# Kernel tuning notes

Measured on AMD Instinct MI355X. Metric: run time of the kernel, lower is better.

## Reference

```python
import jax, jax.numpy as jnp
import numpy as np

ALPHA = 0.5  # leakage
T, B, I, H = 512, 64, 128, 1024
SCALE = 0.9  # input_scaling
RHO = 0.99   # target spectral radius (approximated by 1/sqrt(H) normal scaling)


def setup_inputs() -> dict:
    key = jax.random.key(0)
    k1, k2, k3, k4, k5 = jax.random.split(key, 5)
    x = jax.random.normal(k1, (T, B, I), dtype=jnp.float32)
    # uniform(-scale, scale) kernel init
    W_in0 = jax.random.uniform(k2, (H, I), jnp.float32, -SCALE, SCALE)
    # normal recurrent init scaled so spectral radius ~= rho (circular law: radius ~ sigma*sqrt(H))
    W_hat0 = jax.random.normal(k3, (H, H), jnp.float32) * (RHO / np.sqrt(H))
    W_in1 = jax.random.uniform(k4, (H, H), jnp.float32, -SCALE, SCALE)
    W_hat1 = jax.random.normal(k5, (H, H), jnp.float32) * (RHO / np.sqrt(H))
    return {"x": x, "W_in0": W_in0, "W_hat0": W_hat0, "W_in1": W_in1, "W_hat1": W_hat1}


def _run_layer(inp, W_in, W_hat):
    # inp: [T, B, F_in]; returns full state trajectory [T, B, H]
    def step(h, x_t):
        pre = x_t @ W_in.T + h @ W_hat.T          # [B, H]
        h_new = (1.0 - ALPHA) * h + ALPHA * jnp.tanh(pre)
        return h_new, h_new

    h0 = jnp.zeros((inp.shape[1], W_hat.shape[0]), dtype=inp.dtype)
    _, ys = jax.lax.scan(step, h0, inp)
    return ys


def reference(x, W_in0, W_hat0, W_in1, W_hat1):
    e0 = _run_layer(x, W_in0, W_hat0)   # layer 0 states [T, B, H]
    e1 = _run_layer(e0, W_in1, W_hat1)  # layer 1 states [T, B, H]
    return jnp.stack([e0, e1], axis=-2)  # [T, B, num_layers, H]
```

## Files before the change

### kernel.cpp

```cpp
#include <hip/hip_runtime.h>
#include <math.h>

#define TSTEPS 512
#define BATCH  64
#define HDIM   1024
#define IDIM   128
#define NBLOCKS 256
#define NTHR   512

typedef __attribute__((ext_vector_type(8))) short bf16x8;
typedef __attribute__((ext_vector_type(4))) float f32x4;
typedef __attribute__((ext_vector_type(4))) unsigned u32x4;

#define WI0HI 0
#define WI0LO (WI0HI + 1024*128)
#define WH0HI (WI0LO + 1024*128)
#define WH0LO (WH0HI + 1024*1024)
#define WI1HI (WH0LO + 1024*1024)
#define WI1LO (WI1HI + 1024*1024)
#define WH1HI (WI1LO + 1024*1024)
#define WH1LO (WH1HI + 1024*1024)
#define WS_USHORTS (WH1LO + 1024*1024)
#define CNT_OFF_BYTES ((size_t)WS_USHORTS * 2)
#define BAR_BYTES (256 * 64)

__device__ __forceinline__ unsigned short bf_hi(float f) {
    unsigned u = __builtin_bit_cast(unsigned, f);
    unsigned r = u + 0x7fffu + ((u >> 16) & 1u);
    return (unsigned short)(r >> 16);
}
__device__ __forceinline__ float bf_tof(unsigned short h) {
    unsigned u = ((unsigned)h) << 16;
    return __builtin_bit_cast(float, u);
}

__device__ __forceinline__ void split8v(f32x4 a, f32x4 b,
                                        bf16x8& ah, bf16x8& al) {
    float fv[8] = {a[0], a[1], a[2], a[3], b[0], b[1], b[2], b[3]};
    u32x4 H, L;
    #pragma unroll
    for (int q = 0; q < 4; ++q) {
        const float f0 = fv[2 * q], f1 = fv[2 * q + 1];
        unsigned h;
        asm("v_cvt_pk_bf16_f32 %0, %1, %2" : "=v"(h) : "v"(f0), "v"(f1));
        const float h0 = __builtin_bit_cast(float, h << 16);
        const float h1 = __builtin_bit_cast(float, h & 0xffff0000u);
        unsigned lo;
        asm("v_cvt_pk_bf16_f32 %0, %1, %2" : "=v"(lo) : "v"(f0 - h0), "v"(f1 - h1));
        H[q] = h; L[q] = lo;
    }
    ah = __builtin_bit_cast(bf16x8, H);
    al = __builtin_bit_cast(bf16x8, L);
}

__device__ __forceinline__ void ks_r2(f32x4 a, f32x4 b,
                                      bf16x8 bh, bf16x8 bl, f32x4& acc) {
    bf16x8 ah, al;
    split8v(a, b, ah, al);
    acc = __builtin_amdgcn_mfma_f32_16x16x32_bf16(ah, bh, acc, 0, 0, 0);
    acc = __builtin_amdgcn_mfma_f32_16x16x32_bf16(al, bh, acc, 0, 0, 0);
    acc = __builtin_amdgcn_mfma_f32_16x16x32_bf16(ah, bl, acc, 0, 0, 0);
}

#define LD2(B, base, g) _Pragma("unroll") for (int c = 0; c < 2; ++c) { \
    (B)[2*c]   = *(const f32x4*)((base) + ((g)*2 + c) * 32); \
    (B)[2*c+1] = *(const f32x4*)((base) + ((g)*2 + c) * 32 + 4); }
#define PR2(B, wOff, g) _Pragma("unroll") for (int c = 0; c < 2; ++c) { \
    ks_r2((B)[2*c], (B)[2*c+1], wfh[(wOff)+(g)*2+c], wfl[(wOff)+(g)*2+c], \
          ((((g)*2+c) & 1) ? accA : accB)); }

__global__ void prep_kernel(const float* __restrict__ Wi0, const float* __restrict__ Wh0,
                            const float* __restrict__ Wi1, const float* __restrict__ Wh1,
                            unsigned short* __restrict__ wsU)
{
    const int n = 1024*128 + 3*1024*1024;
    for (int e = blockIdx.x * blockDim.x + threadIdx.x; e < n;
         e += gridDim.x * blockDim.x) {
        const float* src; int idx, hiOff, loOff;
        if (e < 1024*128)            { src = Wi0; idx = e;              hiOff = WI0HI; loOff = WI0LO; }
        else if (e < 1024*128 + 1024*1024)   { src = Wh0; idx = e - 1024*128;   hiOff = WH0HI; loOff = WH0LO; }
        else if (e < 1024*128 + 2*1024*1024) { src = Wi1; idx = e - 1024*128 - 1024*1024; hiOff = WI1HI; loOff = WI1LO; }
        else                         { src = Wh1; idx = e - 1024*128 - 2*1024*1024; hiOff = WH1HI; loOff = WH1LO; }
        float f = src[idx];
        unsigned short h = bf_hi(f);
        wsU[hiOff + idx] = h;
        wsU[loOff + idx] = bf_hi(f - bf_tof(h));
    }
}

__device__ __forceinline__ void barrier_arrive(unsigned* cnt, unsigned epoch,
                                               int dom, int jt) {
    __syncthreads();
    if (threadIdx.x == 0)
        __hip_atomic_store(cnt + (unsigned)(dom * 64 + jt) * 16, epoch,
                           __ATOMIC_RELAXED, __HIP_MEMORY_SCOPE_AGENT);
}
__device__ __forceinline__ void barrier_wait(unsigned* cnt, unsigned epoch,
                                             int layer, int mh) {
    const int tid = (int)threadIdx.x;
    if (tid < 64) {
        const int dom = layer * 2 + mh;
        unsigned* own = cnt + (unsigned)(dom * 64 + tid) * 16;
        if (layer == 0) {
            for (;;) {
                unsigned v = __hip_atomic_load(own, __ATOMIC_RELAXED,
                                               __HIP_MEMORY_SCOPE_AGENT);
                if (__ballot(v >= epoch) == ~0ull) break;
                __builtin_amdgcn_s_sleep(1);
            }
        } else {
            unsigned* up = cnt + (unsigned)(mh * 64 + tid) * 16;
            for (;;) {
                unsigned a = __hip_atomic_load(own, __ATOMIC_RELAXED,
                                               __HIP_MEMORY_SCOPE_AGENT);
                unsigned b = __hip_atomic_load(up, __ATOMIC_RELAXED,
                                               __HIP_MEMORY_SCOPE_AGENT);
                if (__ballot((a >= epoch) & (b >= epoch)) == ~0ull) break;
                __builtin_amdgcn_s_sleep(1);
            }
        }
    }
    __syncthreads();
}

__global__ __launch_bounds__(NTHR, 2) void reservoir_kernel(
    const float* __restrict__ x, float* __restrict__ out,
    const unsigned short* __restrict__ wsU, unsigned* __restrict__ cnt)
{
    __shared__ f32x4 red[8 * 64];

    const int bid = blockIdx.x;
    const int layer = bid >> 7;
    const int rr  = bid & 127;
    const int jt  = rr >> 1, mh = rr & 1;
    const int dom = layer * 2 + mh;
    const int tid = (int)threadIdx.x;
    const int w   = __builtin_amdgcn_readfirstlane(tid >> 6);
    const int m2  = w & 1, kh = w >> 1;
    const int l   = tid & 63, lr = l & 15, tq = l >> 4;
    const int jbase = jt * 16;
    const int arow  = mh * 32 + m2 * 16 + lr;

    bf16x8 wfh[16], wfl[16];
    if (layer == 0) {
        const size_t rx = (size_t)(jbase + lr) * IDIM + kh * 32 + tq * 8;
        wfh[0] = *(const bf16x8*)(wsU + WI0HI + rx);
        wfl[0] = *(const bf16x8*)(wsU + WI0LO + rx);
        const size_t rh = (size_t)(jbase + lr) * HDIM + kh * 256 + tq * 8;
        #pragma unroll
        for (int ks = 0; ks < 8; ++ks) {
            wfh[1 + ks] = *(const bf16x8*)(wsU + WH0HI + rh + ks * 32);
            wfl[1 + ks] = *(const bf16x8*)(wsU + WH0LO + rh + ks * 32);
        }
    } else {
        const int hiOff = (kh < 2) ? WI1HI : WH1HI;
        const int loOff = (kh < 2) ? WI1LO : WH1LO;
        const size_t ro = (size_t)(jbase + lr) * HDIM + (kh & 1) * 512 + tq * 8;
        #pragma unroll
        for (int ks = 0; ks < 16; ++ks) {
            wfh[ks] = *(const bf16x8*)(wsU + hiOff + ro + ks * 32);
            wfl[ks] = *(const bf16x8*)(wsU + loOff + ro + ks * 32);
        }
    }

    const int rowLocal = tid >> 4;
    const int colF = tid & 15;
    const int m2f = rowLocal >> 4, tqf = (rowLocal >> 2) & 3, rf = rowLocal & 3;
    const int lf  = tqf * 16 + colF;
    float hold = 0.f;
    f32x4 accX = {0.f, 0.f, 0.f, 0.f};

    for (int i = 0; i <= TSTEPS; ++i) {
        const int t = layer ? (i - 1) : i;
        const bool valid = layer ? (t >= 0) : (t < TSTEPS);
        if (valid) {
            f32x4 accA = {0.f, 0.f, 0.f, 0.f};
            f32x4 accB = {0.f, 0.f, 0.f, 0.f};
            if (layer == 0) {
                if (i == 0) {
                    f32x4 xa = *(const f32x4*)(x + (size_t)t * (BATCH * IDIM) + arow * IDIM + kh * 32 + tq * 8);
                    f32x4 xb = *(const f32x4*)(x + (size_t)t * (BATCH * IDIM) + arow * IDIM + kh * 32 + tq * 8 + 4);
                    ks_r2(xa, xb, wfh[0], wfl[0], accA);
                } else {
                    accA = accX;
                }
                if (t >= 1) {
                    const float* h0 = out + (size_t)(t - 1) * 131072 + arow * 2048
                                      + kh * 256 + tq * 8;
                    f32x4 bA[4], bB[4];
                    LD2(bA, h0, 0); LD2(bB, h0, 1);
                    PR2(bA, 1, 0); LD2(bA, h0, 2);
                    PR2(bB, 1, 1); LD2(bB, h0, 3);
                    PR2(bA, 1, 2); PR2(bB, 1, 3);
                }
            } else {
                if ((kh < 2) || (t >= 1)) {
                    const int ts  = (kh < 2) ? t : (t - 1);
                    const float* src = out + (size_t)ts * 131072 + arow * 2048
                                       + ((kh < 2) ? 0 : 1024) + (kh & 1) * 512 + tq * 8;
                    f32x4 bA[4], bB[4];
                    LD2(bA, src, 0); LD2(bB, src, 1);
                    PR2(bA, 0, 0); LD2(bA, src, 2);
                    PR2(bB, 0, 1); LD2(bB, src, 3);
                    PR2(bA, 0, 2); LD2(bA, src, 4);
                    PR2(bB, 0, 3); LD2(bB, src, 5);
                    PR2(bA, 0, 4); LD2(bA, src, 6);
                    PR2(bB, 0, 5); LD2(bB, src, 7);
                    PR2(bA, 0, 6); PR2(bB, 0, 7);
                }
            }

            red[w * 64 + l] = accA + accB;
            __syncthreads();
            {
                float s = 0.f;
                #pragma unroll
                for (int k4 = 0; k4 < 4; ++k4)
                    s += red[(k4 * 2 + m2f) * 64 + lf][rf];
                const float hnew = 0.5f * hold + 0.5f * tanhf(s);
                hold = hnew;
                const int row = mh * 32 + rowLocal;
                float* dst = out + (size_t)t * 131072 + row * 2048 + layer * 1024 + jbase + colF;
                __hip_atomic_store(dst, hnew, __ATOMIC_RELAXED, __HIP_MEMORY_SCOPE_AGENT);
            }
            __syncthreads();
        }
        if (i < TSTEPS) {
            barrier_arrive(cnt, (unsigned)(i + 1), dom, jt);
            if (layer == 0 && (i + 1) < TSTEPS) {
                const float* xs = x + (size_t)(i + 1) * (BATCH * IDIM) + arow * IDIM + kh * 32 + tq * 8;
                f32x4 xa = *(const f32x4*)(xs);
                f32x4 xb = *(const f32x4*)(xs + 4);
                f32x4 z = {0.f, 0.f, 0.f, 0.f};
                ks_r2(xa, xb, wfh[0], wfl[0], z);
                accX = z;
            }
            barrier_wait(cnt, (unsigned)(i + 1), layer, mh);
        }
    }
}

extern "C" void kernel_launch(void* const* d_in, const int* in_sizes, int n_in,
                              void* d_out, int out_size, void* d_ws, size_t ws_size,
                              hipStream_t stream) {
    const float* x   = (const float*)d_in[0];
    const float* Wi0 = (const float*)d_in[1];
    const float* Wh0 = (const float*)d_in[2];
    const float* Wi1 = (const float*)d_in[3];
    const float* Wh1 = (const float*)d_in[4];
    float* out = (float*)d_out;
    unsigned short* wsU = (unsigned short*)d_ws;
    unsigned* cnt = (unsigned*)((char*)d_ws + CNT_OFF_BYTES);

    hipMemsetAsync((char*)d_ws + CNT_OFF_BYTES, 0, BAR_BYTES, stream);
    prep_kernel<<<256, 256, 0, stream>>>(Wi0, Wh0, Wi1, Wh1, wsU);

    void* args[] = {(void*)&x, (void*)&out, (void*)&wsU, (void*)&cnt};
    hipLaunchCooperativeKernel((const void*)reservoir_kernel,
                               dim3(NBLOCKS), dim3(NTHR), args, 0, stream);
}
```

Baseline: 4.408 ms.

## Replace block-wide grid barrier with per-wave waits on only the needed producer flags

The old scheme had one wavefront per block poll every producer flag in its domain and then release the whole block with a __syncthreads. Now each wave polls only the 16 or 32 flags for the column slice it actually reads, right before loading it. The x-projection for the next step is no longer precomputed during the barrier; it is computed inline at the start of each step. The intent is to remove the full-block wait and let waves start as soon as their own inputs are ready, at the cost of more polling traffic from many waves and a relaxed-ordering assumption for visibility of the data.

```diff
diff --git a/kernel.cpp b/kernel.cpp
--- a/kernel.cpp
+++ b/kernel.cpp
@@ -88,39 +88,15 @@
     }
 }
 
-__device__ __forceinline__ void barrier_arrive(unsigned* cnt, unsigned epoch,
-                                               int dom, int jt) {
-    __syncthreads();
-    if (threadIdx.x == 0)
-        __hip_atomic_store(cnt + (unsigned)(dom * 64 + jt) * 16, epoch,
-                           __ATOMIC_RELAXED, __HIP_MEMORY_SCOPE_AGENT);
-}
-__device__ __forceinline__ void barrier_wait(unsigned* cnt, unsigned epoch,
-                                             int layer, int mh) {
-    const int tid = (int)threadIdx.x;
-    if (tid < 64) {
-        const int dom = layer * 2 + mh;
-        unsigned* own = cnt + (unsigned)(dom * 64 + tid) * 16;
-        if (layer == 0) {
-            for (;;) {
-                unsigned v = __hip_atomic_load(own, __ATOMIC_RELAXED,
-                                               __HIP_MEMORY_SCOPE_AGENT);
-                if (__ballot(v >= epoch) == ~0ull) break;
-                __builtin_amdgcn_s_sleep(1);
-            }
-        } else {
-            unsigned* up = cnt + (unsigned)(mh * 64 + tid) * 16;
-            for (;;) {
-                unsigned a = __hip_atomic_load(own, __ATOMIC_RELAXED,
-                                               __HIP_MEMORY_SCOPE_AGENT);
-                unsigned b = __hip_atomic_load(up, __ATOMIC_RELAXED,
-                                               __HIP_MEMORY_SCOPE_AGENT);
-                if (__ballot((a >= epoch) & (b >= epoch)) == ~0ull) break;
-                __builtin_amdgcn_s_sleep(1);
-            }
-        }
-    }
-    __syncthreads();
+__device__ __forceinline__ void wave_wait(unsigned* cnt, unsigned epoch,
+                                          int baseLine, int mask) {
+    const int lane = (int)(threadIdx.x & 63);
+    unsigned* p = cnt + (unsigned)(baseLine + (lane & mask)) * 16;
+    for (;;) {
+        unsigned v = __hip_atomic_load(p, __ATOMIC_RELAXED, __HIP_MEMORY_SCOPE_AGENT);
+        if (__ballot(v >= epoch) == ~0ull) break;
+        __builtin_amdgcn_s_sleep(1);
+    }
 }
 
 __global__ __launch_bounds__(NTHR, 2) void reservoir_kernel(
@@ -168,7 +144,6 @@
     const int m2f = rowLocal >> 4, tqf = (rowLocal >> 2) & 3, rf = rowLocal & 3;
     const int lf  = tqf * 16 + colF;
     float hold = 0.f;
-    f32x4 accX = {0.f, 0.f, 0.f, 0.f};
 
     for (int i = 0; i <= TSTEPS; ++i) {
         const int t = layer ? (i - 1) : i;
@@ -177,14 +152,12 @@
             f32x4 accA = {0.f, 0.f, 0.f, 0.f};
             f32x4 accB = {0.f, 0.f, 0.f, 0.f};
             if (layer == 0) {
-                if (i == 0) {
-                    f32x4 xa = *(const f32x4*)(x + (size_t)t * (BATCH * IDIM) + arow * IDIM + kh * 32 + tq * 8);
-                    f32x4 xb = *(const f32x4*)(x + (size_t)t * (BATCH * IDIM) + arow * IDIM + kh * 32 + tq * 8 + 4);
-                    ks_r2(xa, xb, wfh[0], wfl[0], accA);
-                } else {
-                    accA = accX;
+                {
+                    const float* xs = x + (size_t)t * (BATCH * IDIM) + arow * IDIM + kh * 32 + tq * 8;
+                    ks_r2(*(const f32x4*)xs, *(const f32x4*)(xs + 4), wfh[0], wfl[0], accA);
                 }
                 if (t >= 1) {
+                    wave_wait(cnt, (unsigned)i, mh * 64 + kh * 16, 15);
                     const float* h0 = out + (size_t)(t - 1) * 131072 + arow * 2048
                                       + kh * 256 + tq * 8;
                     f32x4 bA[4], bB[4];
@@ -196,6 +169,9 @@
             } else {
                 if ((kh < 2) || (t >= 1)) {
                     const int ts  = (kh < 2) ? t : (t - 1);
+                    const int pbase = (kh < 2) ? (mh * 64 + kh * 32)
+                                               : ((2 + mh) * 64 + (kh - 2) * 32);
+                    wave_wait(cnt, (unsigned)i, pbase, 31);
                     const float* src = out + (size_t)ts * 131072 + arow * 2048
                                        + ((kh < 2) ? 0 : 1024) + (kh & 1) * 512 + tq * 8;
                     f32x4 bA[4], bB[4];
@@ -223,19 +199,13 @@
                 float* dst = out + (size_t)t * 131072 + row * 2048 + layer * 1024 + jbase + colF;
                 __hip_atomic_store(dst, hnew, __ATOMIC_RELAXED, __HIP_MEMORY_SCOPE_AGENT);
             }
+        }
+        if (i < TSTEPS) {
             __syncthreads();
-        }
-        if (i < TSTEPS) {
-            barrier_arrive(cnt, (unsigned)(i + 1), dom, jt);
-            if (layer == 0 && (i + 1) < TSTEPS) {
-                const float* xs = x + (size_t)(i + 1) * (BATCH * IDIM) + arow * IDIM + kh * 32 + tq * 8;
-                f32x4 xa = *(const f32x4*)(xs);
-                f32x4 xb = *(const f32x4*)(xs + 4);
-                f32x4 z = {0.f, 0.f, 0.f, 0.f};
-                ks_r2(xa, xb, wfh[0], wfl[0], z);
-                accX = z;
-            }
-            barrier_wait(cnt, (unsigned)(i + 1), layer, mh);
+            if (tid == 0)
+                __hip_atomic_store(cnt + (unsigned)(dom * 64 + jt) * 16,
+                                   (unsigned)(i + 1),
+                                   __ATOMIC_RELAXED, __HIP_MEMORY_SCOPE_AGENT);
         }
     }
 }
```

Result: faster. 4.208 ms (-4.5%).
